# Optimization experiments

Hardware: AMD Instinct MI355X
Metric: run time of the kernel (lower is better)

Reference implementation:

```python
import jax, jax.numpy as jnp
import numpy as np

DIM = 1024
NUM_HEADS = 16
HEAD_DIM = DIM // NUM_HEADS
SCALE = HEAD_DIM ** -0.5


def setup_inputs() -> dict:
    key = jax.random.key(0)
    k1, k2, k3, k4, k5, k6 = jax.random.split(key, 6)
    B, S, L = 4, 8192, 512
    x = jax.random.normal(k1, (B, S, DIM), dtype=jnp.float32)
    latents = jax.random.normal(k2, (B, L, DIM), dtype=jnp.float32)
    # Linear weights stored torch-style as (out_features, in_features)
    w_q = jax.random.normal(k3, (DIM, DIM), dtype=jnp.float32) * (DIM ** -0.5)
    w_kv = jax.random.normal(k4, (2 * DIM, DIM), dtype=jnp.float32) * (DIM ** -0.5)
    w_out = jax.random.normal(k5, (DIM, DIM), dtype=jnp.float32) * (DIM ** -0.5)
    b_out = jax.random.normal(k6, (DIM,), dtype=jnp.float32) * 0.01
    return {"x": x, "latents": latents, "w_q": w_q, "w_kv": w_kv,
            "w_out": w_out, "b_out": b_out}


def reference(x, latents, w_q, w_kv, w_out, b_out):
    B, L, _ = latents.shape
    S = x.shape[1]
    q = latents @ w_q.T                      # (B, L, dim)
    kv = x @ w_kv.T                          # (B, S, 2*dim)
    k, v = jnp.split(kv, 2, axis=-1)         # each (B, S, dim)
    q = q.reshape(B, L, NUM_HEADS, HEAD_DIM)
    k = k.reshape(B, S, NUM_HEADS, HEAD_DIM)
    v = v.reshape(B, S, NUM_HEADS, HEAD_DIM)
    # attention scores: (B, H, L, S)
    attn = jnp.einsum('blhd,bshd->bhls', q, k) * SCALE
    attn = jax.nn.softmax(attn, axis=-1)
    out = jnp.einsum('bhls,bshd->blhd', attn, v)  # (B, L, H, D)
    out = out.reshape(B, L, DIM)
    return out @ w_out.T + b_out
```

## Files before the change

kernel.cpp:

```cpp
#include <hip/hip_runtime.h>
#include <hip/hip_bf16.h>
#include <cstdint>
#include <cstddef>

#define B_ 4
#define S_ 8192
#define L_ 512
#define DIM 1024
#define NUM_HEADS 16
#define HEAD_DIM 64
#define SCHUNK 4096
#define NSEG 2
#define SEGKEYS (SCHUNK / NSEG)
#define SCALE 0.125f
#define L2E 1.44269504088896f
#define F_SC (SCALE * L2E)

#define XCH (B_ * SCHUNK * DIM / 8)
#define LATCH (B_ * L_ * DIM / 8)
#define WQCH (DIM * DIM / 8)
#define WKVCH (2 * DIM * DIM / 8)

typedef __bf16 bf16;
typedef __bf16 bf16x8 __attribute__((ext_vector_type(8)));
typedef float f32x4 __attribute__((ext_vector_type(4)));

#define AS1 __attribute__((address_space(1)))
#define AS3 __attribute__((address_space(3)))
#define GLDS(g, l) __builtin_amdgcn_global_load_lds((const AS1 void*)(g), (AS3 void*)(l), 16, 0, 0)
#define LGKM_FENCE() asm volatile("s_waitcnt lgkmcnt(0)" ::: "memory")
#define VMCNT4() asm volatile("s_waitcnt vmcnt(4)" ::: "memory")
#define VMCNT0() asm volatile("s_waitcnt vmcnt(0)" ::: "memory")
#define MFMA16(a, b, c) __builtin_amdgcn_mfma_f32_16x16x32_bf16((a), (b), (c), 0, 0, 0)

__device__ __forceinline__ bool detect_f32(const void* xp) {
  const unsigned int* x = (const unsigned int*)xp;
  int cnt = 0;
#pragma unroll
  for (int i = 0; i < 32; ++i) {
    unsigned int e = (x[i] >> 7) & 0xFFu;
    cnt += (e >= 117u && e <= 129u) ? 1 : 0;
  }
  return cnt < 16;
}

__device__ __forceinline__ void conv_chunk(
    const void* in, bf16* out, size_t gc, size_t oc, bool f32in) {
  if (f32in) {
    const f32x4* g = (const f32x4*)in + gc * 2;
    f32x4 lo = g[0], hi = g[1];
    bf16x8 w;
    w[0] = (bf16)lo[0]; w[1] = (bf16)lo[1]; w[2] = (bf16)lo[2]; w[3] = (bf16)lo[3];
    w[4] = (bf16)hi[0]; w[5] = (bf16)hi[1]; w[6] = (bf16)hi[2]; w[7] = (bf16)hi[3];
    *(bf16x8*)(out + oc * 8) = w;
  } else {
    *(bf16x8*)(out + oc * 8) = ((const bf16x8*)in)[gc];
  }
}

__global__ __launch_bounds__(256) void conv_all(
    const void* __restrict__ x, const void* __restrict__ lat,
    const void* __restrict__ wq, const void* __restrict__ wkv,
    bf16* __restrict__ xcb, bf16* __restrict__ latb,
    bf16* __restrict__ wqb, bf16* __restrict__ wkvb)
{
  const bool f32in = detect_f32(x);
  const int TOT = XCH + LATCH + WQCH + WKVCH;
  for (int c = blockIdx.x * 256 + threadIdx.x; c < TOT; c += gridDim.x * 256) {
    if (c < XCH) {
      int r = c >> 7, cc = c & 127;
      size_t gc = ((size_t)((r >> 12) * 8192 + (r & 4095)) << 7) + cc;
      conv_chunk(x, xcb, gc, (size_t)c, f32in);
    } else if (c < XCH + LATCH) {
      int k = c - XCH;
      conv_chunk(lat, latb, (size_t)k, (size_t)k, f32in);
    } else if (c < XCH + LATCH + WQCH) {
      int k = c - XCH - LATCH;
      conv_chunk(wq, wqb, (size_t)k, (size_t)k, f32in);
    } else {
      int k = c - XCH - LATCH - WQCH;
      conv_chunk(wkv, wkvb, (size_t)k, (size_t)k, f32in);
    }
  }
}

template<int HAS_BIAS, int DUAL_OUT, int NBN>
__global__ __launch_bounds__(256) void gemm_nt(
    const bf16* __restrict__ Ap, const bf16* __restrict__ Bwp,
    void* __restrict__ Cp, const void* __restrict__ biasp,
    int M, int N, int K, const void* __restrict__ xdet)
{
  __shared__ __align__(16) bf16 lA[128 * 64];
  __shared__ __align__(16) bf16 lB[128 * 64];
  const int tid = threadIdx.x;
  const int lane = tid & 63, quad = lane >> 4, l16 = lane & 15, wave = tid >> 6;
  const int wm = wave >> 1, wn = wave & 1;
  const int f = blockIdx.x;
  const int xcd = f & 7, sidx = f >> 3;
  const int bn = sidx % NBN;
  const int bm = xcd * (M >> 10) + sidx / NBN;
  const bool f32in = (HAS_BIAS || DUAL_OUT) ? detect_f32(xdet) : false;

  f32x4 acc[4][4] = {};
  const int nK = K >> 6;
  for (int kb = 0; kb < nK; ++kb) {
    __syncthreads();
#pragma unroll
    for (int i = 0; i < 4; ++i) {
      int e = i * 256 + tid;
      int row = e >> 3, cp = e & 7, gcp = cp ^ (row & 7);
      const bf16* ga = Ap + (size_t)(bm * 128 + row) * K + kb * 64 + gcp * 8;
      GLDS(ga, lA + e * 8);
      const bf16* gb = Bwp + (size_t)(bn * 128 + row) * K + kb * 64 + gcp * 8;
      GLDS(gb, lB + e * 8);
    }
    __syncthreads();

#pragma unroll
    for (int ks = 0; ks < 2; ++ks) {
      bf16x8 af[4], bfr[4];
#pragma unroll
      for (int t = 0; t < 4; ++t) {
        int rowA = wm * 64 + t * 16 + l16;
        int ca = (ks * 4 + quad) ^ (rowA & 7);
        af[t] = *(const bf16x8*)(lA + rowA * 64 + ca * 8);
        int rowB = wn * 64 + t * 16 + l16;
        int cb = (ks * 4 + quad) ^ (rowB & 7);
        bfr[t] = *(const bf16x8*)(lB + rowB * 64 + cb * 8);
      }
#pragma unroll
      for (int tm = 0; tm < 4; ++tm)
#pragma unroll
        for (int tn = 0; tn < 4; ++tn)
          acc[tm][tn] = MFMA16(af[tm], bfr[tn], acc[tm][tn]);
    }
  }

#pragma unroll
  for (int tn = 0; tn < 4; ++tn) {
    int col = bn * 128 + wn * 64 + tn * 16 + l16;
    float bv = 0.0f;
    if (HAS_BIAS)
      bv = f32in ? ((const float*)biasp)[col] : (float)((const bf16*)biasp)[col];
#pragma unroll
    for (int tm = 0; tm < 4; ++tm) {
#pragma unroll
      for (int r = 0; r < 4; ++r) {
        int rowc = bm * 128 + wm * 64 + tm * 16 + quad * 4 + r;
        float v = acc[tm][tn][r] + bv;
        if (DUAL_OUT && f32in) {
          ((float*)Cp)[(size_t)rowc * N + col] = v;
        } else {
          ((bf16*)Cp)[(size_t)rowc * N + col] = (bf16)v;
        }
      }
    }
  }
}

__global__ __launch_bounds__(512) void gemm_kv_256(
    const bf16* __restrict__ Ap, const bf16* __restrict__ Bwp,
    bf16* __restrict__ Cp, bf16* __restrict__ C2p, int M, int K)
{
  __shared__ __align__(16) bf16 lA[2][256 * 64];
  __shared__ __align__(16) bf16 lB[2][256 * 64];
  const int tid = threadIdx.x;
  const int lane = tid & 63, quad = lane >> 4, l16 = lane & 15, wave = tid >> 6;
  const int wm = wave >> 2, wn = wave & 3;
  const int f = blockIdx.x;
  const int xcd = f & 7, sidx = f >> 3;
  const int bn = sidx & 7;
  const int bm = xcd * ((M >> 8) >> 3) + (sidx >> 3);
  const int nK = K >> 6;

#define STAGE_A(buf, half, kb) do {                                          \
  _Pragma("unroll")                                                          \
  for (int j = 0; j < 2; ++j) {                                              \
    int e = j * 512 + tid;                                                   \
    int row = e >> 3, cp = e & 7, gcp = cp ^ (row & 7);                      \
    const bf16* g = Ap + (size_t)(bm * 256 + (half) * 128 + row) * K         \
                       + (kb) * 64 + gcp * 8;                                \
    GLDS(g, &lA[buf][((half) * 128 + row) * 64 + cp * 8]);                   \
  } } while (0)
#define STAGE_B(buf, half, kb) do {                                          \
  _Pragma("unroll")                                                          \
  for (int j = 0; j < 2; ++j) {                                              \
    int e = j * 512 + tid;                                                   \
    int row = e >> 3, cp = e & 7, gcp = cp ^ (row & 7);                      \
    const bf16* g = Bwp + (size_t)(bn * 256 + (half) * 128 + row) * K        \
                        + (kb) * 64 + gcp * 8;                               \
    GLDS(g, &lB[buf][((half) * 128 + row) * 64 + cp * 8]);                   \
  } } while (0)

  f32x4 acc[8][4] = {};

  STAGE_A(0, 0, 0); STAGE_A(0, 1, 0); STAGE_B(0, 0, 0); STAGE_B(0, 1, 0);
  if (nK > 1) { STAGE_B(1, 0, 1); STAGE_B(1, 1, 1); VMCNT4(); }
  else VMCNT0();
  __builtin_amdgcn_s_barrier();

  for (int t = 0; t < nK; ++t) {
    const int cur = t & 1;
    bf16x8 breg[4][2];
#pragma unroll
    for (int p = 0; p < 4; ++p) {
      bf16x8 af[2][2];
      if (p == 0) {
#pragma unroll
        for (int nf = 0; nf < 4; ++nf)
#pragma unroll
          for (int ks = 0; ks < 2; ++ks) {
            int rowB = wn * 64 + nf * 16 + l16;
            int cb = (ks * 4 + quad) ^ (rowB & 7);
            breg[nf][ks] = *(const bf16x8*)&lB[cur][rowB * 64 + cb * 8];
          }
      }
#pragma unroll
      for (int mf2 = 0; mf2 < 2; ++mf2)
#pragma unroll
        for (int ks = 0; ks < 2; ++ks) {
          int rowA = wm * 128 + (p * 2 + mf2) * 16 + l16;
          int ca = (ks * 4 + quad) ^ (rowA & 7);
          af[mf2][ks] = *(const bf16x8*)&lA[cur][rowA * 64 + ca * 8];
        }
      LGKM_FENCE();

      if (p == 0) { if (t + 1 < nK) STAGE_A(cur ^ 1, 0, t + 1); }
      else if (p == 1) { if (t + 1 < nK) STAGE_A(cur ^ 1, 1, t + 1); }
      else if (p == 2) { if (t + 2 < nK) STAGE_B(cur, 0, t + 2); }
      else             { if (t + 2 < nK) STAGE_B(cur, 1, t + 2); }

      __builtin_amdgcn_s_barrier();

      __builtin_amdgcn_s_setprio(1);
#pragma unroll
      for (int mf2 = 0; mf2 < 2; ++mf2)
#pragma unroll
        for (int nf = 0; nf < 4; ++nf)
#pragma unroll
          for (int ks = 0; ks < 2; ++ks)
            acc[p * 2 + mf2][nf] = MFMA16(af[mf2][ks], breg[nf][ks], acc[p * 2 + mf2][nf]);
      __builtin_amdgcn_s_setprio(0);
    }
    if (t + 1 < nK) {
      if (t + 2 < nK) VMCNT4(); else VMCNT0();
      __builtin_amdgcn_s_barrier();
    }
  }

#pragma unroll
  for (int tn = 0; tn < 4; ++tn) {
    int col = bn * 256 + wn * 64 + tn * 16 + l16;
    bf16* outp = (col < 1024) ? Cp : C2p;
    int ocol = col & 1023;
#pragma unroll
    for (int tm = 0; tm < 8; ++tm)
#pragma unroll
      for (int r = 0; r < 4; ++r) {
        int rowc = bm * 256 + wm * 128 + tm * 16 + quad * 4 + r;
        outp[(size_t)rowc * 1024 + ocol] = (bf16)acc[tm][tn][r];
      }
  }
#undef STAGE_A
#undef STAGE_B
}

template<int FIRST>
__global__ __launch_bounds__(512) void attn_pass(
    const bf16* __restrict__ qb, const bf16* __restrict__ kc, const bf16* __restrict__ vc,
    float* __restrict__ Ost, float* __restrict__ lst,
    const void* __restrict__ x, bf16* __restrict__ xcb, int srow0)
{
  __shared__ __align__(16) bf16 lK[128 * 64];
  __shared__ __align__(16) bf16 lV[64][136];
  __shared__ __align__(16) bf16 pbuf[8][16][136];

  if (blockIdx.x >= 512) {
    const bool f32in = detect_f32(x);
    const int nb = gridDim.x - 512;
    for (int c = (blockIdx.x - 512) * 512 + threadIdx.x; c < XCH; c += nb * 512) {
      int r = c >> 7, cc = c & 127;
      size_t gc = ((size_t)((r >> 12) * 8192 + srow0 + (r & 4095)) << 7) + cc;
      conv_chunk(x, xcb, gc, (size_t)c, f32in);
    }
    return;
  }

  const int tid = threadIdx.x;
  const int lane = tid & 63, quad = lane >> 4, l16 = lane & 15, wave = tid >> 6;
  const int f = blockIdx.x;
  const int xcd = f & 7, sidx = f >> 3;
  const int lt = sidx & 3, ghi = sidx >> 2;
  const int g = ghi * 8 + xcd;
  const int h = g & 15, bs = g >> 4;
  const int b = bs >> 1, seg = bs & 1;
  const int l0 = lt * 128 + wave * 16;

  const bf16* qbase = qb + (size_t)(b * L_ + l0 + l16) * DIM + h * HEAD_DIM + quad * 8;
  bf16x8 qf0 = *(const bf16x8*)qbase;
  bf16x8 qf1 = *(const bf16x8*)(qbase + 32);

  f32x4 acc[4] = {};
  float lsum[4] = {0.0f, 0.0f, 0.0f, 0.0f};

  const int sbeg = seg * SEGKEYS;
  for (int s0 = sbeg; s0 < sbeg + SEGKEYS; s0 += 128) {
    __syncthreads();
#pragma unroll
    for (int i = 0; i < 2; ++i) {
      int e = i * 512 + tid;
      int row = e >> 3, cp = e & 7, gcp = cp ^ (row & 7);
      const bf16* gk = kc + (size_t)(b * SCHUNK + s0 + row) * DIM + h * HEAD_DIM + gcp * 8;
      GLDS(gk, lK + e * 8);
    }
#pragma unroll
    for (int i = 0; i < 2; ++i) {
      int e = i * 512 + tid;
      int row = e >> 3, cc = e & 7;
      bf16x8 vv = *(const bf16x8*)(vc + (size_t)(b * SCHUNK + s0 + row) * DIM + h * HEAD_DIM + cc * 8);
      int pg = (row >> 3) ^ cc;
#pragma unroll
      for (int j = 0; j < 8; ++j)
        lV[cc * 8 + j][pg * 8 + (row & 7)] = vv[j];
    }
    __syncthreads();

#pragma unroll
    for (int kt = 0; kt < 8; ++kt) {
      int rk = kt * 16 + l16;
      int p0c = quad ^ (rk & 7);
      int p1c = (4 + quad) ^ (rk & 7);
      bf16x8 kf0 = *(const bf16x8*)(lK + rk * 64 + p0c * 8);
      bf16x8 kf1 = *(const bf16x8*)(lK + rk * 64 + p1c * 8);
      f32x4 s4 = {};
      s4 = MFMA16(qf0, kf0, s4);
      s4 = MFMA16(qf1, kf1, s4);
#pragma unroll
      for (int r = 0; r < 4; ++r) {
        float a = exp2f(fminf(s4[r] * F_SC, 40.0f));
        lsum[r] += a;
        pbuf[wave][quad * 4 + r][kt * 16 + l16] = (bf16)a;
      }
    }
    LGKM_FENCE();
#pragma unroll
    for (int half = 0; half < 4; ++half) {
      bf16x8 pf = *(const bf16x8*)&pbuf[wave][l16][half * 32 + quad * 8];
#pragma unroll
      for (int t4 = 0; t4 < 4; ++t4) {
        int c = t4 * 16 + l16;
        int pg = (half * 4 + quad) ^ (c >> 3);
        bf16x8 vf = *(const bf16x8*)&lV[c][pg * 8];
        acc[t4] = MFMA16(pf, vf, acc[t4]);
      }
    }
  }

#pragma unroll
  for (int r = 0; r < 4; ++r) {
    lsum[r] += __shfl_xor(lsum[r], 1, 16);
    lsum[r] += __shfl_xor(lsum[r], 2, 16);
    lsum[r] += __shfl_xor(lsum[r], 4, 16);
    lsum[r] += __shfl_xor(lsum[r], 8, 16);
  }

  float* Oseg = Ost + (size_t)seg * (B_ * L_ * DIM);
  float* lseg = lst + (size_t)seg * (B_ * NUM_HEADS * L_);
#pragma unroll
  for (int r = 0; r < 4; ++r) {
    int l = l0 + quad * 4 + r;
    if (l16 == 0) {
      int si = (b * NUM_HEADS + h) * L_ + l;
      if (FIRST) lseg[si] = lsum[r];
      else       lseg[si] += lsum[r];
    }
  }
#pragma unroll
  for (int t4 = 0; t4 < 4; ++t4)
#pragma unroll
    for (int r = 0; r < 4; ++r) {
      int l = l0 + quad * 4 + r;
      size_t oi = (size_t)(b * L_ + l) * DIM + h * HEAD_DIM + t4 * 16 + l16;
      if (FIRST) Oseg[oi] = acc[t4][r];
      else       Oseg[oi] += acc[t4][r];
    }
}

__global__ __launch_bounds__(256) void combine_wout(
    const float* __restrict__ Ost, const float* __restrict__ lst, bf16* __restrict__ ao,
    const void* __restrict__ x, const void* __restrict__ wout, bf16* __restrict__ woutb)
{
  if (blockIdx.x >= 2048) {
    const bool f32in = detect_f32(x);
    const int nb = gridDim.x - 2048;
    for (int c = (blockIdx.x - 2048) * 256 + threadIdx.x; c < WQCH; c += nb * 256)
      conv_chunk(wout, woutb, (size_t)c, (size_t)c, f32in);
    return;
  }
  int idx = (blockIdx.x * 256 + threadIdx.x) * 4;
  int d0 = idx & (DIM - 1);
  int row = idx >> 10;
  int b = row >> 9, l = row & (L_ - 1);
  int h = d0 >> 6;
  int si = (b * NUM_HEADS + h) * L_ + l;
  float lv = lst[si] + lst[B_ * NUM_HEADS * L_ + si];
  float linv = 1.0f / lv;
  f32x4 o0 = *(const f32x4*)(Ost + idx);
  f32x4 o1 = *(const f32x4*)(Ost + (size_t)(B_ * L_ * DIM) + idx);
#pragma unroll
  for (int j = 0; j < 4; ++j)
    ao[idx + j] = (bf16)((o0[j] + o1[j]) * linv);
}

extern "C" void kernel_launch(void* const* d_in, const int* in_sizes, int n_in,
                              void* d_out, int out_size, void* d_ws, size_t ws_size,
                              hipStream_t stream)
{
  (void)in_sizes; (void)n_in; (void)out_size; (void)ws_size;
  const void* x       = d_in[0];
  const void* latents = d_in[1];
  const void* w_q     = d_in[2];
  const void* w_kv    = d_in[3];
  const void* w_out   = d_in[4];
  const void* b_out   = d_in[5];

  char* ws = (char*)d_ws;
  bf16*  qb    = (bf16*)(ws + ((size_t)1   << 20));
  float* lst   = (float*)(ws + ((size_t)5  << 20));
  bf16*  ao    = (bf16*)(ws + ((size_t)6   << 20));
  float* Ost   = (float*)(ws + ((size_t)10 << 20));
  bf16*  kc    = (bf16*)(ws + ((size_t)26 << 20));
  bf16*  latb  = (bf16*)(ws + ((size_t)26 << 20));
  bf16*  wqb   = (bf16*)(ws + ((size_t)30 << 20));
  bf16*  vc    = (bf16*)(ws + ((size_t)58 << 20));
  bf16*  xcb   = (bf16*)(ws + ((size_t)90 << 20));
  bf16*  wkvb  = (bf16*)(ws + ((size_t)122 << 20));
  bf16*  woutb = (bf16*)(ws + ((size_t)122 << 20));

  const int Mx = B_ * SCHUNK;

  conv_all<<<2048, 256, 0, stream>>>(x, latents, w_q, w_kv, xcb, latb, wqb, wkvb);

  gemm_nt<0, 0, 8><<<128, 256, 0, stream>>>(
      latb, wqb, qb, nullptr, B_ * L_, DIM, DIM, x);

  gemm_kv_256<<<512, 512, 0, stream>>>(xcb, wkvb, kc, vc, Mx, DIM);

  attn_pass<1><<<1024, 512, 0, stream>>>(qb, kc, vc, Ost, lst, x, xcb, SCHUNK);

  gemm_kv_256<<<512, 512, 0, stream>>>(xcb, wkvb, kc, vc, Mx, DIM);

  attn_pass<0><<<512, 512, 0, stream>>>(qb, kc, vc, Ost, lst, x, xcb, 0);

  combine_wout<<<2560, 256, 0, stream>>>(Ost, lst, ao, x, w_out, woutb);

  gemm_nt<1, 1, 8><<<128, 256, 0, stream>>>(
      ao, woutb, d_out, b_out, B_ * L_, DIM, DIM, x);
}
```

Measured before the change: 557.2 us.

## Fuse Q projection into KV GEMM launch and compute softmax row sums via MFMA

```diff
diff --git a/kernel.cpp b/kernel.cpp
--- a/kernel.cpp
+++ b/kernel.cpp
@@ -84,7 +84,7 @@
   }
 }
 
-template<int HAS_BIAS, int DUAL_OUT, int NBN>
+template<int NBN>
 __global__ __launch_bounds__(256) void gemm_nt(
     const bf16* __restrict__ Ap, const bf16* __restrict__ Bwp,
     void* __restrict__ Cp, const void* __restrict__ biasp,
@@ -99,7 +99,7 @@
   const int xcd = f & 7, sidx = f >> 3;
   const int bn = sidx % NBN;
   const int bm = xcd * (M >> 10) + sidx / NBN;
-  const bool f32in = (HAS_BIAS || DUAL_OUT) ? detect_f32(xdet) : false;
+  const bool f32in = detect_f32(xdet);
 
   f32x4 acc[4][4] = {};
   const int nK = K >> 6;
@@ -139,33 +139,85 @@
 #pragma unroll
   for (int tn = 0; tn < 4; ++tn) {
     int col = bn * 128 + wn * 64 + tn * 16 + l16;
-    float bv = 0.0f;
-    if (HAS_BIAS)
-      bv = f32in ? ((const float*)biasp)[col] : (float)((const bf16*)biasp)[col];
+    float bv = f32in ? ((const float*)biasp)[col] : (float)((const bf16*)biasp)[col];
 #pragma unroll
     for (int tm = 0; tm < 4; ++tm) {
 #pragma unroll
       for (int r = 0; r < 4; ++r) {
         int rowc = bm * 128 + wm * 64 + tm * 16 + quad * 4 + r;
         float v = acc[tm][tn][r] + bv;
-        if (DUAL_OUT && f32in) {
-          ((float*)Cp)[(size_t)rowc * N + col] = v;
-        } else {
-          ((bf16*)Cp)[(size_t)rowc * N + col] = (bf16)v;
-        }
-      }
-    }
-  }
-}
-
+        if (f32in) ((float*)Cp)[(size_t)rowc * N + col] = v;
+        else       ((bf16*)Cp)[(size_t)rowc * N + col] = (bf16)v;
+      }
+    }
+  }
+}
+
+template<int QF>
 __global__ __launch_bounds__(512) void gemm_kv_256(
     const bf16* __restrict__ Ap, const bf16* __restrict__ Bwp,
-    bf16* __restrict__ Cp, bf16* __restrict__ C2p, int M, int K)
+    bf16* __restrict__ Cp, bf16* __restrict__ C2p, int M, int K,
+    const bf16* __restrict__ Aq, const bf16* __restrict__ Bq,
+    bf16* __restrict__ Cq)
 {
   __shared__ __align__(16) bf16 lA[2][256 * 64];
   __shared__ __align__(16) bf16 lB[2][256 * 64];
   const int tid = threadIdx.x;
   const int lane = tid & 63, quad = lane >> 4, l16 = lane & 15, wave = tid >> 6;
+
+  if (QF && blockIdx.x >= 512) {
+    const int qi = blockIdx.x - 512;
+    const int bm = qi >> 3, bn = qi & 7;
+    const int wm2 = wave >> 2, wn2 = wave & 3;
+    bf16* lAq = lA[0]; bf16* lBq = lB[0];
+    f32x4 qacc[4][2] = {};
+#pragma unroll 1
+    for (int kb = 0; kb < 16; ++kb) {
+      __syncthreads();
+#pragma unroll
+      for (int j = 0; j < 2; ++j) {
+        int e = j * 512 + tid;
+        int row = e >> 3, cp = e & 7, gcp = cp ^ (row & 7);
+        GLDS(Aq + (size_t)(bm * 128 + row) * 1024 + kb * 64 + gcp * 8, lAq + e * 8);
+        GLDS(Bq + (size_t)(bn * 128 + row) * 1024 + kb * 64 + gcp * 8, lBq + e * 8);
+      }
+      __syncthreads();
+#pragma unroll
+      for (int ks = 0; ks < 2; ++ks) {
+        bf16x8 af[4], bfr[2];
+#pragma unroll
+        for (int t = 0; t < 4; ++t) {
+          int rowA = wm2 * 64 + t * 16 + l16;
+          int ca = (ks * 4 + quad) ^ (rowA & 7);
+          af[t] = *(const bf16x8*)(lAq + rowA * 64 + ca * 8);
+        }
+#pragma unroll
+        for (int u = 0; u < 2; ++u) {
+          int rowB = wn2 * 32 + u * 16 + l16;
+          int cb = (ks * 4 + quad) ^ (rowB & 7);
+          bfr[u] = *(const bf16x8*)(lBq + rowB * 64 + cb * 8);
+        }
+#pragma unroll
+        for (int t = 0; t < 4; ++t)
+#pragma unroll
+          for (int u = 0; u < 2; ++u)
+            qacc[t][u] = MFMA16(af[t], bfr[u], qacc[t][u]);
+      }
+    }
+#pragma unroll
+    for (int u = 0; u < 2; ++u) {
+      int col = bn * 128 + wn2 * 32 + u * 16 + l16;
+#pragma unroll
+      for (int t = 0; t < 4; ++t)
+#pragma unroll
+        for (int r = 0; r < 4; ++r) {
+          int rowc = bm * 128 + wm2 * 64 + t * 16 + quad * 4 + r;
+          Cq[(size_t)rowc * 1024 + col] = (bf16)(qacc[t][u][r] * F_SC);
+        }
+    }
+    return;
+  }
+
   const int wm = wave >> 2, wn = wave & 3;
   const int f = blockIdx.x;
   const int xcd = f & 7, sidx = f >> 3;
@@ -300,8 +352,12 @@
   bf16x8 qf0 = *(const bf16x8*)qbase;
   bf16x8 qf1 = *(const bf16x8*)(qbase + 32);
 
+  bf16x8 vones;
+#pragma unroll
+  for (int j = 0; j < 8; ++j) vones[j] = (bf16)1.0f;
+
   f32x4 acc[4] = {};
-  float lsum[4] = {0.0f, 0.0f, 0.0f, 0.0f};
+  f32x4 accs = {};
 
   const int sbeg = seg * SEGKEYS;
   for (int s0 = sbeg; s0 < sbeg + SEGKEYS; s0 += 128) {
@@ -337,8 +393,7 @@
       s4 = MFMA16(qf1, kf1, s4);
 #pragma unroll
       for (int r = 0; r < 4; ++r) {
-        float a = exp2f(fminf(s4[r] * F_SC, 40.0f));
-        lsum[r] += a;
+        float a = exp2f(fminf(s4[r], 40.0f));
         pbuf[wave][quad * 4 + r][kt * 16 + l16] = (bf16)a;
       }
     }
@@ -346,6 +401,7 @@
 #pragma unroll
     for (int half = 0; half < 4; ++half) {
       bf16x8 pf = *(const bf16x8*)&pbuf[wave][l16][half * 32 + quad * 8];
+      accs = MFMA16(pf, vones, accs);
 #pragma unroll
       for (int t4 = 0; t4 < 4; ++t4) {
         int c = t4 * 16 + l16;
@@ -356,14 +412,6 @@
     }
   }
 
-#pragma unroll
-  for (int r = 0; r < 4; ++r) {
-    lsum[r] += __shfl_xor(lsum[r], 1, 16);
-    lsum[r] += __shfl_xor(lsum[r], 2, 16);
-    lsum[r] += __shfl_xor(lsum[r], 4, 16);
-    lsum[r] += __shfl_xor(lsum[r], 8, 16);
-  }
-
   float* Oseg = Ost + (size_t)seg * (B_ * L_ * DIM);
   float* lseg = lst + (size_t)seg * (B_ * NUM_HEADS * L_);
 #pragma unroll
@@ -371,8 +419,8 @@
     int l = l0 + quad * 4 + r;
     if (l16 == 0) {
       int si = (b * NUM_HEADS + h) * L_ + l;
-      if (FIRST) lseg[si] = lsum[r];
-      else       lseg[si] += lsum[r];
+      if (FIRST) lseg[si] = accs[r];
+      else       lseg[si] += accs[r];
     }
   }
 #pragma unroll
@@ -429,9 +477,9 @@
   float* lst   = (float*)(ws + ((size_t)5  << 20));
   bf16*  ao    = (bf16*)(ws + ((size_t)6   << 20));
   float* Ost   = (float*)(ws + ((size_t)10 << 20));
+  bf16*  latb  = (bf16*)(ws + ((size_t)10 << 20));
+  bf16*  wqb   = (bf16*)(ws + ((size_t)14 << 20));
   bf16*  kc    = (bf16*)(ws + ((size_t)26 << 20));
-  bf16*  latb  = (bf16*)(ws + ((size_t)26 << 20));
-  bf16*  wqb   = (bf16*)(ws + ((size_t)30 << 20));
   bf16*  vc    = (bf16*)(ws + ((size_t)58 << 20));
   bf16*  xcb   = (bf16*)(ws + ((size_t)90 << 20));
   bf16*  wkvb  = (bf16*)(ws + ((size_t)122 << 20));
@@ -441,19 +489,16 @@
 
   conv_all<<<2048, 256, 0, stream>>>(x, latents, w_q, w_kv, xcb, latb, wqb, wkvb);
 
-  gemm_nt<0, 0, 8><<<128, 256, 0, stream>>>(
-      latb, wqb, qb, nullptr, B_ * L_, DIM, DIM, x);
-
-  gemm_kv_256<<<512, 512, 0, stream>>>(xcb, wkvb, kc, vc, Mx, DIM);
+  gemm_kv_256<1><<<640, 512, 0, stream>>>(xcb, wkvb, kc, vc, Mx, DIM, latb, wqb, qb);
 
   attn_pass<1><<<1024, 512, 0, stream>>>(qb, kc, vc, Ost, lst, x, xcb, SCHUNK);
 
-  gemm_kv_256<<<512, 512, 0, stream>>>(xcb, wkvb, kc, vc, Mx, DIM);
+  gemm_kv_256<0><<<512, 512, 0, stream>>>(xcb, wkvb, kc, vc, Mx, DIM, nullptr, nullptr, nullptr);
 
   attn_pass<0><<<512, 512, 0, stream>>>(qb, kc, vc, Ost, lst, x, xcb, 0);
 
   combine_wout<<<2560, 256, 0, stream>>>(Ost, lst, ao, x, w_out, woutb);
 
-  gemm_nt<1, 1, 8><<<128, 256, 0, stream>>>(
+  gemm_nt<8><<<128, 256, 0, stream>>>(
       ao, woutb, d_out, b_out, B_ * L_, DIM, DIM, x);
 }
```

Result: no change. 547.9 us (-1.7%).
